# Kernel tuning notes

Measured on AMD Instinct MI355X. Metric: run time of the kernel, lower is better.

The kernel has to match this reference:

```python
import jax, jax.numpy as jnp
import numpy as np

BS, N_CH, H, R, N_AGGR, T = 32768, 16, 128, 64, 4, 128


def _xavier(key, shape):
    fan_in, fan_out = shape[-2], shape[-1]
    lim = float(np.sqrt(6.0 / (fan_in + fan_out)))
    return jax.random.uniform(key, shape, jnp.float32, -lim, lim)


def setup_inputs() -> dict:
    key = jax.random.key(0)
    ks = jax.random.split(key, 9)
    return {
        "neighbour_h": jax.random.normal(ks[0], (BS, N_CH, H), jnp.float32),
        "type_embs": jax.random.normal(ks[1], (BS, T), jnp.float32),
        "A": _xavier(ks[2], (N_AGGR, H, R)),
        "B": _xavier(ks[3], (N_AGGR, R, R)),
        "A_b": _xavier(ks[4], (N_AGGR, 1, R)),
        "U_type": _xavier(ks[5], (N_AGGR, T, R)),
        "b_type": _xavier(ks[6], (N_AGGR, 1, R)),
        "U_output": _xavier(ks[7], (N_AGGR, R, H)),
        "b_output": _xavier(ks[8], (N_AGGR, 1, H)),
    }


def reference(neighbour_h, type_embs, A, B, A_b, U_type, b_type, U_output, b_output):
    bs = neighbour_h.shape[0]
    # per-child input projection: (bs, n_ch, n_aggr, rank)
    ris = jnp.einsum('bch,ahr->bcar', neighbour_h, A) + A_b[:, 0]
    # initial state from node-type embedding: (bs, n_aggr, rank)
    r0 = jnp.einsum('bt,atr->bar', type_embs, U_type) + b_type[:, 0]
    # linear recurrence over children: r_t = r_{t-1} @ B + a_t
    a_seq = jnp.moveaxis(ris, 1, 0)  # (n_ch, bs, n_aggr, rank)

    def step(r, a_t):
        return jnp.einsum('bar,arq->baq', r, B) + a_t, None

    r_fin, _ = jax.lax.scan(step, r0, a_seq)
    # output projection: (bs, n_aggr, h_size)
    out = jnp.einsum('bar,arh->bah', r_fin, U_output) + b_output[:, 0]
    return out.reshape(bs, -1)
```

## Files before the change

### kernel.cpp

```cpp
#include <hip/hip_runtime.h>
#include <hip/hip_bf16.h>


typedef short bf16x8 __attribute__((ext_vector_type(8)));
typedef float f32x4  __attribute__((ext_vector_type(4)));

__device__ __forceinline__ unsigned f2bfbits(float f) {
    unsigned u = __builtin_bit_cast(unsigned, f);
    return (u + 0x7FFFu + ((u >> 16) & 1u)) >> 16;
}
__device__ __forceinline__ unsigned pack2(float a, float b) {
    unsigned lo = (unsigned)__builtin_bit_cast(unsigned short, __float2bfloat16(a));
    unsigned hi = (unsigned)__builtin_bit_cast(unsigned short, __float2bfloat16(b));
    return lo | (hi << 16);
}

#define SYNC_NODRAIN() do {                                   \
    asm volatile("s_waitcnt lgkmcnt(0)" ::: "memory");        \
    __builtin_amdgcn_s_barrier();                             \
} while (0)

#define FS 68

__global__ __launch_bounds__(512) void tt_fold(
    const float* __restrict__ Ag,
    const float* __restrict__ Bg,
    const float* __restrict__ Abg,
    const float* __restrict__ Utg,
    const float* __restrict__ btg,
    const float* __restrict__ Uog,
    const float* __restrict__ bog,
    unsigned short* __restrict__ Wp,
    float* __restrict__ biasOut)
{
    __shared__ __align__(16) float L[23552];
    const int t = threadIdx.x;
    const int bid = blockIdx.x;

    auto mm = [&](float* d, const float* x, const float* y, const float* add) {
        const int r = t >> 3, c0 = (t & 7) << 3;
        float acc[8];
#pragma unroll
        for (int j = 0; j < 8; ++j) acc[j] = 0.f;
        for (int k = 0; k < 64; ++k) {
            const float a = x[r * FS + k];
            const float4 y0 = *(const float4*)(y + k * FS + c0);
            const float4 y1 = *(const float4*)(y + k * FS + c0 + 4);
            acc[0] += a * y0.x; acc[1] += a * y0.y;
            acc[2] += a * y0.z; acc[3] += a * y0.w;
            acc[4] += a * y1.x; acc[5] += a * y1.y;
            acc[6] += a * y1.z; acc[7] += a * y1.w;
        }
        if (add) {
#pragma unroll
            for (int j = 0; j < 8; ++j) acc[j] += add[r * FS + c0 + j];
        }
#pragma unroll
        for (int j = 0; j < 8; ++j) d[r * FS + c0 + j] = acc[j];
    };

    float* buf[4];
    buf[0] = L;
    buf[1] = L + 4352;
    buf[2] = L + 8704;
    buf[3] = L + 13056;
    float* const Pbuf = L + 17408;
    float* const UC   = L + 21504;

    if (bid < 68) {
        int a, p, kbase;
        const float* src;
        if (bid < 64) { a = bid >> 4; const int c = bid & 15; p = 15 - c; kbase = c * 128; src = Ag  + a * 8192; }
        else          { a = bid - 64; p = 16; kbase = 2048;               src = Utg + a * 8192; }
        const float* Bmat = Bg + a * 4096;

        for (int i = t; i < 4096; i += 512) {
            const int row = i >> 6, col = i & 63;
            buf[0][row * FS + col] = Bmat[i];
            buf[2][row * FS + col] = (row == col) ? 1.f : 0.f;
        }
        __syncthreads();
        int bcur = 0, rcur = 2;
        int e = p;
        while (e) {
            if (e & 1) { mm(buf[rcur ^ 1], buf[rcur], buf[bcur], nullptr); rcur ^= 1; __syncthreads(); }
            e >>= 1;
            if (e)     { mm(buf[bcur ^ 1], buf[bcur], buf[bcur], nullptr); bcur ^= 1; __syncthreads(); }
        }

        {
            const int prow = t >> 3, pc0 = (t & 7) << 3;
#pragma unroll
            for (int j = 0; j < 8; ++j)
                Pbuf[prow * 64 + pc0 + j] = buf[rcur][prow * FS + pc0 + j];
        }
        __syncthreads();

        float* M1 = L;
        {
            const int i = t >> 2, r0 = (t & 3) << 4;
            float acc[16];
#pragma unroll
            for (int j = 0; j < 16; ++j) acc[j] = 0.f;
            for (int q = 0; q < 64; ++q) {
                const float av = src[i * 64 + q];
                const float4* pr = (const float4*)(Pbuf + q * 64 + r0);
#pragma unroll
                for (int jj = 0; jj < 4; ++jj) {
                    float4 v = pr[jj];
                    acc[4 * jj + 0] += av * v.x;
                    acc[4 * jj + 1] += av * v.y;
                    acc[4 * jj + 2] += av * v.z;
                    acc[4 * jj + 3] += av * v.w;
                }
            }
#pragma unroll
            for (int j = 0; j < 16; ++j) M1[i * 65 + r0 + j] = acc[j];
        }
        __syncthreads();

        const float* UoA = Uog + a * 8192;
        const int i = t >> 2, h0 = (t & 3) << 5;
        float acc2[32];
#pragma unroll
        for (int j = 0; j < 32; ++j) acc2[j] = 0.f;
        for (int ch = 0; ch < 4; ++ch) {
            __syncthreads();
            for (int idx = t; idx < 2048; idx += 512) UC[idx] = UoA[ch * 2048 + idx];
            __syncthreads();
            for (int rr = 0; rr < 16; ++rr) {
                const float m = M1[i * 65 + ch * 16 + rr];
                const float4* ur = (const float4*)(UC + rr * 128 + h0);
#pragma unroll
                for (int jj = 0; jj < 8; ++jj) {
                    float4 v = ur[jj];
                    acc2[4 * jj + 0] += m * v.x;
                    acc2[4 * jj + 1] += m * v.y;
                    acc2[4 * jj + 2] += m * v.z;
                    acc2[4 * jj + 3] += m * v.w;
                }
            }
        }
        {
            const int k = kbase + i;
            const int kt = k >> 6, slot = (k >> 3) & 7, widx = k & 7;
#pragma unroll
            for (int j = 0; j < 32; ++j) {
                const int n = a * 128 + h0 + j;
                Wp[((size_t)(kt * 8 + slot) * 512 + n) * 8 + widx] =
                    (unsigned short)f2bfbits(acc2[j]);
            }
        }
    } else {
        const int a = bid - 68;
        const float* Bmat = Bg + a * 4096;
        for (int i = t; i < 4096; i += 512) {
            const int row = i >> 6, col = i & 63;
            buf[0][row * FS + col] = Bmat[i];
            buf[2][row * FS + col] = (row == col) ? 1.f : 0.f;
        }
        __syncthreads();
        int bcur = 0, scur = 2;
        for (int rnd = 0; rnd < 4; ++rnd) {
            mm(buf[scur ^ 1], buf[bcur], buf[scur], buf[scur]);
            mm(buf[bcur ^ 1], buf[bcur], buf[bcur], nullptr);
            __syncthreads();
            scur ^= 1; bcur ^= 1;
        }
        float* vv = Pbuf;
        if (t < 64) {
            float acc = 0.f;
            const float* S16 = buf[scur];
            const float* B16 = buf[bcur];
            for (int q = 0; q < 64; ++q)
                acc += Abg[a * 64 + q] * S16[q * FS + t]
                     + btg[a * 64 + q] * B16[q * FS + t];
            vv[t] = acc;
        }
        __syncthreads();
        if (t < 128) {
            float accb = bog[a * 128 + t];
            const float* UoA = Uog + a * 8192;
            for (int r = 0; r < 64; ++r) accb += vv[r] * UoA[r * 128 + t];
            biasOut[a * 128 + t] = accb;
        }
    }
}
#undef FS

__global__ __launch_bounds__(256) void tt_gemm(
    const float* __restrict__ nh,
    const float* __restrict__ te,
    const unsigned short* __restrict__ Wp,
    const float* __restrict__ bias,
    float* __restrict__ out)
{
    __shared__ __align__(16) char Ab[16384];

    const int t = threadIdx.x;
    const int lane = t & 63, wave = t >> 6;
    const int lt = (blockIdx.x & 7) * 128 + (blockIdx.x >> 3);
    const int m0 = (lt >> 1) * 64;
    const int wc = (lt & 1) * 4 + wave;
    const int lx = lane & 15, lg = lane >> 4;

    const int r = t >> 2, c = t & 3;
    const float* nhp = nh + (size_t)(m0 + r) * 2048 + c * 16;
    const float* tep = te + (size_t)(m0 + r) * 128  + c * 16;
    const int awoff = (c >> 1) * 4096 + (c & 1) * 2048 + r * 16;
    const int aroff = lg * 1024 + lx * 16;

    const char* const wbase = (const char*)Wp + lg * 8192 + wc * 1024 + lx * 16;

    f32x4 acc[4][4] = {};
    float4 va0[4], va1[4];
    uint4  bF0[4][2], bF1[4][2];

#define LOADA(dst, kt_) do {                                                   \
    const float* _p = ((kt_) < 32) ? (nhp + (kt_) * 64) : (tep + ((kt_) - 32) * 64); \
    _Pragma("unroll")                                                          \
    for (int _j = 0; _j < 4; ++_j) dst[_j] = *(const float4*)(_p + 4 * _j);    \
} while (0)

#define WRITEA(src, d_) do {                                                   \
    uint4 _w0, _w1;                                                            \
    _w0.x = pack2(src[0].x, src[0].y);  _w0.y = pack2(src[0].z, src[0].w);     \
    _w0.z = pack2(src[1].x, src[1].y);  _w0.w = pack2(src[1].z, src[1].w);     \
    _w1.x = pack2(src[2].x, src[2].y);  _w1.y = pack2(src[2].z, src[2].w);     \
    _w1.z = pack2(src[3].x, src[3].y);  _w1.w = pack2(src[3].z, src[3].w);     \
    *(uint4*)(Ab + (d_) * 8192 + awoff)        = _w0;                          \
    *(uint4*)(Ab + (d_) * 8192 + awoff + 1024) = _w1;                          \
} while (0)

#define LOADB(dst, kt_) do {                                                   \
    const char* _q = wbase + (size_t)(kt_) * 65536;                            \
    _Pragma("unroll")                                                          \
    for (int _kk = 0; _kk < 2; ++_kk)                                          \
        _Pragma("unroll")                                                      \
        for (int _fn = 0; _fn < 4; ++_fn)                                      \
            dst[_fn][_kk] = *(const uint4*)(_q + _kk * 32768 + _fn * 256);     \
} while (0)

#define COMPUTE(d_, bsrc) do {                                                 \
    _Pragma("unroll")                                                          \
    for (int _kk = 0; _kk < 2; ++_kk) {                                        \
        bf16x8 _aF[4];                                                         \
        _Pragma("unroll")                                                      \
        for (int _fm = 0; _fm < 4; ++_fm)                                      \
            _aF[_fm] = *(const bf16x8*)(Ab + (d_) * 8192 + _kk * 4096 + aroff + _fm * 256); \
        _Pragma("unroll")                                                      \
        for (int _fm = 0; _fm < 4; ++_fm)                                      \
            _Pragma("unroll")                                                  \
            for (int _fn = 0; _fn < 4; ++_fn)                                  \
                acc[_fm][_fn] = __builtin_amdgcn_mfma_f32_16x16x32_bf16(       \
                    _aF[_fm], __builtin_bit_cast(bf16x8, bsrc[_fn][_kk]),      \
                    acc[_fm][_fn], 0, 0, 0);                                   \
    }                                                                          \
} while (0)

    LOADA(va0, 0);
    WRITEA(va0, 0);
    LOADA(va1, 1);
    LOADA(va0, 2);
    LOADB(bF0, 0);
    LOADB(bF1, 1);
    SYNC_NODRAIN();

#pragma unroll 1
    for (int kt = 0; kt < 34; kt += 2) {
        WRITEA(va1, 1);
        if (kt + 3 < 34) LOADA(va1, kt + 3);
        COMPUTE(0, bF0);
        if (kt + 2 < 34) LOADB(bF0, kt + 2);
        SYNC_NODRAIN();

        if (kt + 2 < 34) {
            WRITEA(va0, 0);
            if (kt + 4 < 34) LOADA(va0, kt + 4);
        }
        COMPUTE(1, bF1);
        if (kt + 3 < 34) LOADB(bF1, kt + 3);
        SYNC_NODRAIN();
    }
#undef LOADA
#undef WRITEA
#undef LOADB
#undef COMPUTE

    const int orow = m0 + lg * 4;
    const int ocol = wc * 64 + lx;
    float bv[4];
#pragma unroll
    for (int fn = 0; fn < 4; ++fn) bv[fn] = bias[ocol + fn * 16];
#pragma unroll
    for (int fm = 0; fm < 4; ++fm)
#pragma unroll
        for (int fn = 0; fn < 4; ++fn)
#pragma unroll
            for (int j = 0; j < 4; ++j)
                out[(size_t)(orow + fm * 16 + j) * 512 + ocol + fn * 16] =
                    acc[fm][fn][j] + bv[fn];
}

extern "C" void kernel_launch(void* const* d_in, const int* in_sizes, int n_in,
                              void* d_out, int out_size, void* d_ws, size_t ws_size,
                              hipStream_t stream) {
    const float* nh  = (const float*)d_in[0];
    const float* te  = (const float*)d_in[1];
    const float* Ag  = (const float*)d_in[2];
    const float* Bg  = (const float*)d_in[3];
    const float* Abg = (const float*)d_in[4];
    const float* Utg = (const float*)d_in[5];
    const float* btg = (const float*)d_in[6];
    const float* Uog = (const float*)d_in[7];
    const float* bog = (const float*)d_in[8];

    unsigned short* Wp = (unsigned short*)d_ws;
    float* bias = (float*)((char*)d_ws + (size_t)34 * 8 * 512 * 8 * 2);
    float* out = (float*)d_out;

    hipLaunchKernelGGL(tt_fold, dim3(72), dim3(512), 0, stream,
                       Ag, Bg, Abg, Utg, btg, Uog, bog, Wp, bias);
    hipLaunchKernelGGL(tt_gemm, dim3(1024), dim3(256), 0, stream,
                       nh, te, Wp, bias, out);
}
```

Before: 201.2 us.

## Load A fragments directly into registers, dropping LDS staging and barriers

The GEMM kernel no longer stages the fp32 activation tile through shared memory. Each wave now loads its own rows from global memory straight into MFMA fragment layout, converts them to bf16 in registers, and needs no block barriers. Blocks double to 512 threads, covering 128 rows, to compensate. This removes LDS traffic and synchronisation, but it loses the cross-thread A reuse. Each of the four column waves now reads the same A rows redundantly from global or L2, with less latency hiding because A loads are no longer prefetched ahead.

Measured after the change: 382.8 us. 90.2% more time.

```diff
diff --git a/kernel.cpp b/kernel.cpp
--- a/kernel.cpp
+++ b/kernel.cpp
@@ -14,11 +14,6 @@
     unsigned hi = (unsigned)__builtin_bit_cast(unsigned short, __float2bfloat16(b));
     return lo | (hi << 16);
 }
-
-#define SYNC_NODRAIN() do {                                   \
-    asm volatile("s_waitcnt lgkmcnt(0)" ::: "memory");        \
-    __builtin_amdgcn_s_barrier();                             \
-} while (0)
 
 #define FS 68
 
@@ -188,49 +183,32 @@
 }
 #undef FS
 
-__global__ __launch_bounds__(256) void tt_gemm(
+__global__ __launch_bounds__(512) void tt_gemm(
     const float* __restrict__ nh,
     const float* __restrict__ te,
     const unsigned short* __restrict__ Wp,
     const float* __restrict__ bias,
     float* __restrict__ out)
 {
-    __shared__ __align__(16) char Ab[16384];
-
     const int t = threadIdx.x;
-    const int lane = t & 63, wave = t >> 6;
-    const int lt = (blockIdx.x & 7) * 128 + (blockIdx.x >> 3);
-    const int m0 = (lt >> 1) * 64;
-    const int wc = (lt & 1) * 4 + wave;
+    const int lane = t & 63, w = t >> 6;
+    const int lt = (blockIdx.x & 7) * 64 + (blockIdx.x >> 3);
+    const int m0 = (lt >> 1) * 128 + (w >> 2) * 64;
+    const int wc = (lt & 1) * 4 + (w & 3);
     const int lx = lane & 15, lg = lane >> 4;
 
-    const int r = t >> 2, c = t & 3;
-    const float* nhp = nh + (size_t)(m0 + r) * 2048 + c * 16;
-    const float* tep = te + (size_t)(m0 + r) * 128  + c * 16;
-    const int awoff = (c >> 1) * 4096 + (c & 1) * 2048 + r * 16;
-    const int aroff = lg * 1024 + lx * 16;
+    const float* ar[4];
+    const float* trp[4];
+#pragma unroll
+    for (int fm = 0; fm < 4; ++fm) {
+        ar[fm]  = nh + (size_t)(m0 + fm * 16 + lx) * 2048 + lg * 8;
+        trp[fm] = te + (size_t)(m0 + fm * 16 + lx) * 128  + lg * 8;
+    }
 
     const char* const wbase = (const char*)Wp + lg * 8192 + wc * 1024 + lx * 16;
 
     f32x4 acc[4][4] = {};
-    float4 va0[4], va1[4];
     uint4  bF0[4][2], bF1[4][2];
-
-#define LOADA(dst, kt_) do {                                                   \
-    const float* _p = ((kt_) < 32) ? (nhp + (kt_) * 64) : (tep + ((kt_) - 32) * 64); \
-    _Pragma("unroll")                                                          \
-    for (int _j = 0; _j < 4; ++_j) dst[_j] = *(const float4*)(_p + 4 * _j);    \
-} while (0)
-
-#define WRITEA(src, d_) do {                                                   \
-    uint4 _w0, _w1;                                                            \
-    _w0.x = pack2(src[0].x, src[0].y);  _w0.y = pack2(src[0].z, src[0].w);     \
-    _w0.z = pack2(src[1].x, src[1].y);  _w0.w = pack2(src[1].z, src[1].w);     \
-    _w1.x = pack2(src[2].x, src[2].y);  _w1.y = pack2(src[2].z, src[2].w);     \
-    _w1.z = pack2(src[3].x, src[3].y);  _w1.w = pack2(src[3].z, src[3].w);     \
-    *(uint4*)(Ab + (d_) * 8192 + awoff)        = _w0;                          \
-    *(uint4*)(Ab + (d_) * 8192 + awoff + 1024) = _w1;                          \
-} while (0)
 
 #define LOADB(dst, kt_) do {                                                   \
     const char* _q = wbase + (size_t)(kt_) * 65536;                            \
@@ -241,51 +219,45 @@
             dst[_fn][_kk] = *(const uint4*)(_q + _kk * 32768 + _fn * 256);     \
 } while (0)
 
-#define COMPUTE(d_, bsrc) do {                                                 \
+#define ASTEP(kt_, bsrc) do {                                                  \
     _Pragma("unroll")                                                          \
-    for (int _kk = 0; _kk < 2; ++_kk) {                                        \
-        bf16x8 _aF[4];                                                         \
+    for (int _fm = 0; _fm < 4; ++_fm) {                                        \
+        const float* _p = ((kt_) < 32) ? (ar[_fm] + (kt_) * 64)                \
+                                       : (trp[_fm] + ((kt_) - 32) * 64);       \
+        float4 _x0 = *(const float4*)(_p);                                     \
+        float4 _x1 = *(const float4*)(_p + 4);                                 \
+        float4 _x2 = *(const float4*)(_p + 32);                                \
+        float4 _x3 = *(const float4*)(_p + 36);                                \
+        uint4 _u0, _u1;                                                        \
+        _u0.x = pack2(_x0.x, _x0.y);  _u0.y = pack2(_x0.z, _x0.w);             \
+        _u0.z = pack2(_x1.x, _x1.y);  _u0.w = pack2(_x1.z, _x1.w);             \
+        _u1.x = pack2(_x2.x, _x2.y);  _u1.y = pack2(_x2.z, _x2.w);             \
+        _u1.z = pack2(_x3.x, _x3.y);  _u1.w = pack2(_x3.z, _x3.w);             \
+        bf16x8 _a0 = __builtin_bit_cast(bf16x8, _u0);                          \
+        bf16x8 _a1 = __builtin_bit_cast(bf16x8, _u1);                          \
         _Pragma("unroll")                                                      \
-        for (int _fm = 0; _fm < 4; ++_fm)                                      \
-            _aF[_fm] = *(const bf16x8*)(Ab + (d_) * 8192 + _kk * 4096 + aroff + _fm * 256); \
+        for (int _fn = 0; _fn < 4; ++_fn)                                      \
+            acc[_fm][_fn] = __builtin_amdgcn_mfma_f32_16x16x32_bf16(           \
+                _a0, __builtin_bit_cast(bf16x8, bsrc[_fn][0]),                 \
+                acc[_fm][_fn], 0, 0, 0);                                       \
         _Pragma("unroll")                                                      \
-        for (int _fm = 0; _fm < 4; ++_fm)                                      \
-            _Pragma("unroll")                                                  \
-            for (int _fn = 0; _fn < 4; ++_fn)                                  \
-                acc[_fm][_fn] = __builtin_amdgcn_mfma_f32_16x16x32_bf16(       \
-                    _aF[_fm], __builtin_bit_cast(bf16x8, bsrc[_fn][_kk]),      \
-                    acc[_fm][_fn], 0, 0, 0);                                   \
+        for (int _fn = 0; _fn < 4; ++_fn)                                      \
+            acc[_fm][_fn] = __builtin_amdgcn_mfma_f32_16x16x32_bf16(           \
+                _a1, __builtin_bit_cast(bf16x8, bsrc[_fn][1]),                 \
+                acc[_fm][_fn], 0, 0, 0);                                       \
     }                                                                          \
 } while (0)
 
-    LOADA(va0, 0);
-    WRITEA(va0, 0);
-    LOADA(va1, 1);
-    LOADA(va0, 2);
     LOADB(bF0, 0);
-    LOADB(bF1, 1);
-    SYNC_NODRAIN();
-
 #pragma unroll 1
     for (int kt = 0; kt < 34; kt += 2) {
-        WRITEA(va1, 1);
-        if (kt + 3 < 34) LOADA(va1, kt + 3);
-        COMPUTE(0, bF0);
+        LOADB(bF1, kt + 1);
+        ASTEP(kt, bF0);
         if (kt + 2 < 34) LOADB(bF0, kt + 2);
-        SYNC_NODRAIN();
-
-        if (kt + 2 < 34) {
-            WRITEA(va0, 0);
-            if (kt + 4 < 34) LOADA(va0, kt + 4);
-        }
-        COMPUTE(1, bF1);
-        if (kt + 3 < 34) LOADB(bF1, kt + 3);
-        SYNC_NODRAIN();
+        ASTEP(kt + 1, bF1);
     }
-#undef LOADA
-#undef WRITEA
+#undef ASTEP
 #undef LOADB
-#undef COMPUTE
 
     const int orow = m0 + lg * 4;
     const int ocol = wc * 64 + lx;
@@ -321,6 +293,6 @@
 
     hipLaunchKernelGGL(tt_fold, dim3(72), dim3(512), 0, stream,
                        Ag, Bg, Abg, Utg, btg, Uog, bog, Wp, bias);
-    hipLaunchKernelGGL(tt_gemm, dim3(1024), dim3(256), 0, stream,
+    hipLaunchKernelGGL(tt_gemm, dim3(512), dim3(512), 0, stream,
                        nh, te, Wp, bias, out);
 }
```

## Pre-convert activations to packed bf16 and stream tiles via global_load_lds

Applied to the files above, without the earlier changes.

Adds extra blocks to the prep kernel that convert neighbour_h and type_embs from fp32 into a tile-packed bf16 buffer in workspace. A new GEMM kernel streams both A and B tiles straight into LDS with global_load_lds and a three-slot pipeline, using a 128x128 block tile. This halves GEMM-side A reads and drops the in-kernel conversion, but adds a full fp32 read plus bf16 write of the activations in the prep pass. The old path remains as a fallback when the workspace is too small.

Measured after the change: 196.0 us. 1.03x faster.

```diff
diff --git a/kernel.cpp b/kernel.cpp
--- a/kernel.cpp
+++ b/kernel.cpp
@@ -15,14 +15,11 @@
     return lo | (hi << 16);
 }
 
-#define SYNC_NODRAIN() do {                                   \
-    asm volatile("s_waitcnt lgkmcnt(0)" ::: "memory");        \
-    __builtin_amdgcn_s_barrier();                             \
-} while (0)
-
 #define FS 68
 
-__global__ __launch_bounds__(512) void tt_fold(
+__global__ __launch_bounds__(512) void tt_prep(
+    const float* __restrict__ nh,
+    const float* __restrict__ te,
     const float* __restrict__ Ag,
     const float* __restrict__ Bg,
     const float* __restrict__ Abg,
@@ -30,12 +27,37 @@
     const float* __restrict__ btg,
     const float* __restrict__ Uog,
     const float* __restrict__ bog,
-    unsigned short* __restrict__ Wp,
-    float* __restrict__ biasOut)
+    unsigned short* __restrict__ Bp,
+    float* __restrict__ biasOut,
+    unsigned short* __restrict__ Ap)
 {
     __shared__ __align__(16) float L[23552];
     const int t = threadIdx.x;
     const int bid = blockIdx.x;
+
+    if (bid >= 72) {
+        const int cb = bid - 72;
+        const int mt = cb >> 3;
+        const int r = t >> 2, q = t & 3;
+        for (int kt = cb & 7; kt < 34; kt += 8) {
+            const float* src = (kt < 32)
+                ? nh + ((size_t)(mt * 128 + r) * 2048 + kt * 64 + q * 16)
+                : te + ((size_t)(mt * 128 + r) * 128 + (kt - 32) * 64 + q * 16);
+            float4 v0 = ((const float4*)src)[0];
+            float4 v1 = ((const float4*)src)[1];
+            float4 v2 = ((const float4*)src)[2];
+            float4 v3 = ((const float4*)src)[3];
+            uint4 w0, w1;
+            w0.x = pack2(v0.x, v0.y);  w0.y = pack2(v0.z, v0.w);
+            w0.z = pack2(v1.x, v1.y);  w0.w = pack2(v1.z, v1.w);
+            w1.x = pack2(v2.x, v2.y);  w1.y = pack2(v2.z, v2.w);
+            w1.z = pack2(v3.x, v3.y);  w1.w = pack2(v3.z, v3.w);
+            unsigned short* dst = Ap + (size_t)(mt * 34 + kt) * 8192;
+            *(uint4*)(dst + (2 * q)     * 1024 + r * 8) = w0;
+            *(uint4*)(dst + (2 * q + 1) * 1024 + r * 8) = w1;
+        }
+        return;
+    }
 
     auto mm = [&](float* d, const float* x, const float* y, const float* add) {
         const int r = t >> 3, c0 = (t & 7) << 3;
@@ -147,7 +169,7 @@
 #pragma unroll
             for (int j = 0; j < 32; ++j) {
                 const int n = a * 128 + h0 + j;
-                Wp[((size_t)(kt * 8 + slot) * 512 + n) * 8 + widx] =
+                Bp[((size_t)(((n >> 7) * 34 + kt) * 8 + slot)) * 1024 + (n & 127) * 8 + widx] =
                     (unsigned short)f2bfbits(acc2[j]);
             }
         }
@@ -188,10 +210,104 @@
 }
 #undef FS
 
+#define WAITBAR(NSTR) \
+    asm volatile("s_waitcnt vmcnt(" NSTR ")\n\ts_barrier" ::: "memory")
+
 __global__ __launch_bounds__(256) void tt_gemm(
+    const unsigned short* __restrict__ Ap,
+    const unsigned short* __restrict__ Bp,
+    const float* __restrict__ bias,
+    float* __restrict__ out)
+{
+    __shared__ __align__(16) char Lds[49152];
+
+    const int t = threadIdx.x;
+    const int lane = t & 63, w = t >> 6;
+    const int lt = (blockIdx.x & 7) * 128 + (blockIdx.x >> 3);
+    const int mt = lt >> 2, nb = lt & 3;
+    const int wr = w >> 1, wc = w & 1;
+    const int lx = lane & 15, lg = lane >> 4;
+
+    const char* const asrc = (const char*)Ap + (size_t)mt * 557056 + w * 2048 + lane * 16;
+    const char* const bsrc = (const char*)Bp + (size_t)nb * 557056 + w * 2048 + lane * 16;
+
+    const int aro = lg * 2048 + (wr * 64 + lx) * 16;
+    const int bro = lg * 2048 + (wc * 64 + lx) * 16;
+
+    f32x4 acc[4][4] = {};
+
+#define STAGE(slot_, s_) do {                                                  \
+    const char* _ga = asrc + (size_t)(s_) * 8192;                              \
+    const char* _gb = bsrc + (size_t)(s_) * 8192;                              \
+    char* _ld = Lds + (slot_) * 16384 + w * 2048;                              \
+    _Pragma("unroll")                                                          \
+    for (int _j = 0; _j < 2; ++_j)                                             \
+        __builtin_amdgcn_global_load_lds(                                      \
+            (const __attribute__((address_space(1))) unsigned int*)(_ga + _j * 1024), \
+            (__attribute__((address_space(3))) unsigned int*)(_ld + _j * 1024),\
+            16, 0, 0);                                                         \
+    _Pragma("unroll")                                                          \
+    for (int _j = 0; _j < 2; ++_j)                                             \
+        __builtin_amdgcn_global_load_lds(                                      \
+            (const __attribute__((address_space(1))) unsigned int*)(_gb + _j * 1024), \
+            (__attribute__((address_space(3))) unsigned int*)(_ld + 8192 + _j * 1024), \
+            16, 0, 0);                                                         \
+} while (0)
+
+    STAGE(0, 0);
+    STAGE(1, 1);
+    WAITBAR("4");
+
+    int cur = 0;
+#pragma unroll 1
+    for (int s = 0; s < 68; ++s) {
+        const int nxt2 = (cur >= 1) ? cur - 1 : cur + 2;
+        if (s + 2 < 68) STAGE(nxt2, s + 2);
+
+        const char* Ab = Lds + cur * 16384;
+        bf16x8 aF[4], bF[4];
+#pragma unroll
+        for (int f = 0; f < 4; ++f) {
+            aF[f] = *(const bf16x8*)(Ab + aro + f * 256);
+            bF[f] = *(const bf16x8*)(Ab + 8192 + bro + f * 256);
+        }
+#pragma unroll
+        for (int fm = 0; fm < 4; ++fm)
+#pragma unroll
+            for (int fn = 0; fn < 4; ++fn)
+                acc[fm][fn] = __builtin_amdgcn_mfma_f32_16x16x32_bf16(
+                    aF[fm], bF[fn], acc[fm][fn], 0, 0, 0);
+
+        if (s + 2 < 68)      WAITBAR("4");
+        else if (s + 1 < 68) WAITBAR("0");
+        cur = (cur == 2) ? 0 : cur + 1;
+    }
+#undef STAGE
+
+    const int orow = mt * 128 + wr * 64 + lg * 4;
+    const int ocol = nb * 128 + wc * 64 + lx;
+    float bv[4];
+#pragma unroll
+    for (int fn = 0; fn < 4; ++fn) bv[fn] = bias[ocol + fn * 16];
+#pragma unroll
+    for (int fm = 0; fm < 4; ++fm)
+#pragma unroll
+        for (int fn = 0; fn < 4; ++fn)
+#pragma unroll
+            for (int j = 0; j < 4; ++j)
+                out[(size_t)(orow + fm * 16 + j) * 512 + ocol + fn * 16] =
+                    acc[fm][fn][j] + bv[fn];
+}
+
+#define SYNC_NODRAIN() do {                                   \
+    asm volatile("s_waitcnt lgkmcnt(0)" ::: "memory");        \
+    __builtin_amdgcn_s_barrier();                             \
+} while (0)
+
+__global__ __launch_bounds__(256) void tt_gemm_fb(
     const float* __restrict__ nh,
     const float* __restrict__ te,
-    const unsigned short* __restrict__ Wp,
+    const unsigned short* __restrict__ Bp,
     const float* __restrict__ bias,
     float* __restrict__ out)
 {
@@ -210,7 +326,8 @@
     const int awoff = (c >> 1) * 4096 + (c & 1) * 2048 + r * 16;
     const int aroff = lg * 1024 + lx * 16;
 
-    const char* const wbase = (const char*)Wp + lg * 8192 + wc * 1024 + lx * 16;
+    const char* const wbase = (const char*)Bp + (size_t)(wc >> 1) * 557056
+                              + ((wc & 1) * 64 + lx) * 16 + lg * 2048;
 
     f32x4 acc[4][4] = {};
     float4 va0[4], va1[4];
@@ -233,12 +350,12 @@
 } while (0)
 
 #define LOADB(dst, kt_) do {                                                   \
-    const char* _q = wbase + (size_t)(kt_) * 65536;                            \
+    const char* _q = wbase + (size_t)(kt_) * 16384;                            \
     _Pragma("unroll")                                                          \
     for (int _kk = 0; _kk < 2; ++_kk)                                          \
         _Pragma("unroll")                                                      \
         for (int _fn = 0; _fn < 4; ++_fn)                                      \
-            dst[_fn][_kk] = *(const uint4*)(_q + _kk * 32768 + _fn * 256);     \
+            dst[_fn][_kk] = *(const uint4*)(_q + _kk * 8192 + _fn * 256);      \
 } while (0)
 
 #define COMPUTE(d_, bsrc) do {                                                 \
@@ -315,12 +432,22 @@
     const float* Uog = (const float*)d_in[7];
     const float* bog = (const float*)d_in[8];
 
-    unsigned short* Wp = (unsigned short*)d_ws;
-    float* bias = (float*)((char*)d_ws + (size_t)34 * 8 * 512 * 8 * 2);
+    unsigned short* Bp = (unsigned short*)d_ws;
+    float* bias = (float*)((char*)d_ws + 2228224);
+    unsigned short* Ap = (unsigned short*)((char*)d_ws + 2230272);
     float* out = (float*)d_out;
 
-    hipLaunchKernelGGL(tt_fold, dim3(72), dim3(512), 0, stream,
-                       Ag, Bg, Abg, Utg, btg, Uog, bog, Wp, bias);
-    hipLaunchKernelGGL(tt_gemm, dim3(1024), dim3(256), 0, stream,
-                       nh, te, Wp, bias, out);
-}
+    const bool fast = ws_size >= (size_t)144836608;
+
+    if (fast) {
+        hipLaunchKernelGGL(tt_prep, dim3(72 + 2048), dim3(512), 0, stream,
+                           nh, te, Ag, Bg, Abg, Utg, btg, Uog, bog, Bp, bias, Ap);
+        hipLaunchKernelGGL(tt_gemm, dim3(1024), dim3(256), 0, stream,
+                           Ap, Bp, bias, out);
+    } else {
+        hipLaunchKernelGGL(tt_prep, dim3(72), dim3(512), 0, stream,
+                           nh, te, Ag, Bg, Abg, Utg, btg, Uog, bog, Bp, bias, Ap);
+        hipLaunchKernelGGL(tt_gemm_fb, dim3(1024), dim3(256), 0, stream,
+                           nh, te, Bp, bias, out);
+    }
+}
```
